# Performance work log

Hardware: AMD Instinct MI355X
Metric: run time of the kernel (lower is better)

Reference implementation:

```python
import jax, jax.numpy as jnp
import numpy as np

N_NODES = 50000
N_EDGES = 800000
IN_DIM = 128
HID_DIM = 128
OUT_DIM = 128
LEAKY_SLOPE = 0.01  # torch F.leaky_relu default


def setup_inputs() -> dict:
    key = jax.random.key(0)
    ks = jax.random.split(key, 10)
    src = jax.random.randint(ks[0], (N_EDGES,), 0, N_NODES)
    dst = jax.random.randint(ks[1], (N_EDGES,), 0, N_NODES)
    x = jax.random.normal(ks[2], (N_NODES, IN_DIM), dtype=jnp.float32)
    mask = jnp.ones((HID_DIM,), dtype=jnp.float32)
    # GraphConv 1 (in -> hid), with bias (DGL default)
    W1 = jax.random.normal(ks[3], (IN_DIM, HID_DIM), dtype=jnp.float32) * (1.0 / np.sqrt(IN_DIM))
    b1 = jnp.zeros((HID_DIM,), dtype=jnp.float32)
    # BicliqueAttentionLayer (hid -> hid), linear has no bias
    Wa = jax.random.normal(ks[4], (HID_DIM, HID_DIM), dtype=jnp.float32) * (1.0 / np.sqrt(HID_DIM))
    a = jax.random.normal(ks[5], (HID_DIM, 1), dtype=jnp.float32) * (1.414 / np.sqrt(HID_DIM))
    # GraphConv 2 (hid -> out)
    W2 = jax.random.normal(ks[6], (HID_DIM, OUT_DIM), dtype=jnp.float32) * (1.0 / np.sqrt(HID_DIM))
    b2 = jnp.zeros((OUT_DIM,), dtype=jnp.float32)
    return {"src": src, "dst": dst, "x": x, "mask": mask,
            "W1": W1, "b1": b1, "Wa": Wa, "a": a, "W2": W2, "b2": b2}


def _inv_sqrt_deg(idx, n):
    deg = jax.ops.segment_sum(jnp.ones(idx.shape[0], jnp.float32), idx, num_segments=n)
    return jnp.where(deg > 0, jax.lax.rsqrt(jnp.maximum(deg, 1.0)), 0.0)


def _graph_conv(h, src, dst, W, b):
    # DGL GraphConv norm='both': D_out^{-1/2} on src side, aggregate, D_in^{-1/2} on dst side
    n = h.shape[0]
    norm_src = _inv_sqrt_deg(src, n)   # out-degree of source nodes
    norm_dst = _inv_sqrt_deg(dst, n)   # in-degree of destination nodes
    h = (h @ W) * norm_src[:, None]    # project first (same math, smaller if out<in)
    agg = jax.ops.segment_sum(h[src], dst, num_segments=n)  # scatter-sum to dst
    return agg * norm_dst[:, None] + b


def _biclique_attn(h, src, dst, mask, Wa, a):
    n = h.shape[0]
    hm = (h * mask[None, :]) @ Wa                      # [N, hid]
    score_node = jnp.squeeze(hm @ a, -1)               # [N] per-node attn logit
    score = jax.nn.leaky_relu(score_node[src], LEAKY_SLOPE)  # [E]
    # segment softmax keyed by dst
    smax = jax.ops.segment_max(score, dst, num_segments=n)   # -inf for empty segments
    e = jnp.exp(score - smax[dst])
    ssum = jax.ops.segment_sum(e, dst, num_segments=n)
    alpha = e / ssum[dst]                              # [E]
    h_new = jax.ops.segment_sum(hm[src] * alpha[:, None], dst, num_segments=n)
    return jax.nn.relu(h_new)


def reference(src, dst, x, mask, W1, b1, Wa, a, W2, b2):
    h = jax.nn.relu(_graph_conv(x, src, dst, W1, b1))
    h = _biclique_attn(h, src, dst, mask, Wa, a)
    h = jax.nn.relu(_graph_conv(h, src, dst, W2, b2))
    return h
```

## Files before the change

kernel.cpp:

```cpp
#include <hip/hip_runtime.h>
#include <hip/hip_fp16.h>
#include <math.h>

#define NNODES 50000
#define NEDGES 800000
#define DIM 128
#define NCOARSE 196
#define SCHUNK 2048
#define KPAD 136
#define BCAP 6144

static inline int ceil_div(int a, int b){ return (a + b - 1) / b; }

__device__ __forceinline__ float leaky01(float x){ return x > 0.f ? x : 0.01f * x; }

typedef _Float16 f16;
typedef f16 f16x4 __attribute__((ext_vector_type(4)));
typedef f16 f16x8 __attribute__((ext_vector_type(8)));
typedef float f32x4 __attribute__((ext_vector_type(4)));

__global__ void waa_init(const float* __restrict__ Wa, const float* __restrict__ a,
                         const float* __restrict__ mask, float* __restrict__ waam,
                         int* __restrict__ dcur, int* __restrict__ scur){
    int gtid = blockIdx.x * blockDim.x + threadIdx.x;
    if (gtid < NCOARSE){ dcur[gtid] = gtid * BCAP; scur[gtid] = gtid * BCAP; }
    int k = gtid >> 6, lane = threadIdx.x & 63;
    if (k >= DIM) return;
    float2 v  = *(const float2*)(Wa + (long long)k * DIM + lane * 2);
    float2 av = *(const float2*)(a + lane * 2);
    float s = fmaf(v.x, av.x, v.y * av.y);
    #pragma unroll
    for (int off = 32; off > 0; off >>= 1) s += __shfl_down(s, off);
    if (lane == 0) waam[k] = s * mask[k];
}

__global__ __launch_bounds__(256) void coarse_scatter(const int* __restrict__ src,
    const int* __restrict__ dst, int* __restrict__ dcur, int* __restrict__ scur,
    int* __restrict__ dbuf, unsigned char* __restrict__ sbuf, int E)
{
    __shared__ int hist[NCOARSE], loff[NCOARSE], gbase[NCOARSE], cur[NCOARSE];
    __shared__ int ws4[4];
    __shared__ int stage[SCHUNK];
    int t = threadIdx.x;
    int lane = t & 63, w = t >> 6;
    int base = blockIdx.x * SCHUNK;
    int lim = base + SCHUNK < E ? base + SCHUNK : E;
    int cnt = lim - base;

    if (t < NCOARSE) hist[t] = 0;
    __syncthreads();
    for (int i = base + t; i < lim; i += 256)
        atomicAdd(&hist[dst[i] >> 8], 1);
    __syncthreads();
    {
        int v = (t < NCOARSE) ? hist[t] : 0;
        int inc = v;
        #pragma unroll
        for (int d = 1; d < 64; d <<= 1){ int u = __shfl_up(inc, d); if (lane >= d) inc += u; }
        if (lane == 63) ws4[w] = inc;
        __syncthreads();
        if (t == 0){ int r = 0;
            #pragma unroll
            for (int k = 0; k < 4; ++k){ int xx = ws4[k]; ws4[k] = r; r += xx; } }
        __syncthreads();
        if (t < NCOARSE){
            int excl = ws4[w] + inc - v;
            loff[t] = excl; cur[t] = excl;
            gbase[t] = v ? atomicAdd(&dcur[t], v) : 0;
        }
    }
    __syncthreads();
    for (int i = base + t; i < lim; i += 256){
        int d = dst[i], s = src[i];
        int b = d >> 8;
        int pos = atomicAdd(&cur[b], 1);
        stage[pos] = (b << 24) | ((d & 255) << 16) | s;
    }
    __syncthreads();
    for (int i = t; i < cnt; i += 256){
        int v = stage[i];
        int b = (int)((unsigned)v >> 24);
        dbuf[gbase[b] + (i - loff[b])] = v;
    }
    __syncthreads();

    if (t < NCOARSE) hist[t] = 0;
    __syncthreads();
    for (int i = base + t; i < lim; i += 256)
        atomicAdd(&hist[src[i] >> 8], 1);
    __syncthreads();
    {
        int v = (t < NCOARSE) ? hist[t] : 0;
        int inc = v;
        #pragma unroll
        for (int d = 1; d < 64; d <<= 1){ int u = __shfl_up(inc, d); if (lane >= d) inc += u; }
        if (lane == 63) ws4[w] = inc;
        __syncthreads();
        if (t == 0){ int r = 0;
            #pragma unroll
            for (int k = 0; k < 4; ++k){ int xx = ws4[k]; ws4[k] = r; r += xx; } }
        __syncthreads();
        if (t < NCOARSE){
            int excl = ws4[w] + inc - v;
            loff[t] = excl; cur[t] = excl;
            gbase[t] = v ? atomicAdd(&scur[t], v) : 0;
        }
    }
    __syncthreads();
    unsigned short* st16 = (unsigned short*)stage;
    for (int i = base + t; i < lim; i += 256){
        int s = src[i];
        int b = s >> 8;
        int pos = atomicAdd(&cur[b], 1);
        st16[pos] = (unsigned short)((b << 8) | (s & 255));
    }
    __syncthreads();
    for (int i = t; i < cnt; i += 256){
        int v = st16[i];
        int b = v >> 8;
        sbuf[gbase[b] + (i - loff[b])] = (unsigned char)(v & 255);
    }
}

__global__ __launch_bounds__(256) void bucket_all(const int* __restrict__ dbuf,
    const unsigned char* __restrict__ sbuf, const int* __restrict__ dcur,
    const int* __restrict__ scur, int* __restrict__ rbeg, int* __restrict__ rend,
    float* __restrict__ nd, float* __restrict__ ns, unsigned short* __restrict__ csrc)
{
    __shared__ int stage[BCAP];
    __shared__ int h[256], off[256], cur[256];
    __shared__ int ws4[4];
    int t = threadIdx.x;
    int b = blockIdx.x;

    if (b < NCOARSE){
        int beg = b * BCAP, end = dcur[b], cnt = end - beg;
        h[t] = 0; cur[t] = 0;
        __syncthreads();
        for (int i = t; i < cnt; i += 256){
            int v = dbuf[beg + i];
            stage[i] = v;
            atomicAdd(&h[(v >> 16) & 255], 1);
        }
        __syncthreads();
        int v = h[t];
        int lane = t & 63, w = t >> 6, inc = v;
        #pragma unroll
        for (int d = 1; d < 64; d <<= 1){
            int u = __shfl_up(inc, d);
            if (lane >= d) inc += u;
        }
        if (lane == 63) ws4[w] = inc;
        __syncthreads();
        if (t == 0){
            int r = 0;
            #pragma unroll
            for (int k = 0; k < 4; ++k){ int xx = ws4[k]; ws4[k] = r; r += xx; }
        }
        __syncthreads();
        off[t] = ws4[w] + inc - v;
        __syncthreads();
        int d = b * 256 + t;
        if (d < NNODES){
            rbeg[d] = beg + off[t];
            rend[d] = beg + off[t] + v;
            nd[d] = v > 0 ? rsqrtf((float)v) : 0.f;
        }
        for (int i = t; i < cnt; i += 256){
            int pv = stage[i];
            int j = (pv >> 16) & 255;
            int pos = atomicAdd(&cur[j], 1);
            csrc[beg + off[j] + pos] = (unsigned short)(pv & 0xFFFF);
        }
    } else {
        b -= NCOARSE;
        int beg = b * BCAP, end = scur[b];
        h[t] = 0;
        __syncthreads();
        for (int i = beg + t; i < end; i += 256)
            atomicAdd(&h[sbuf[i]], 1);
        __syncthreads();
        int s = b * 256 + t;
        if (s < NNODES) ns[s] = h[t] > 0 ? rsqrtf((float)h[t]) : 0.f;
    }
}

template<typename TIN, bool USE_MASK, bool USE_ROWSCALE>
__global__ __launch_bounds__(256) void gemm_mfma(const TIN* __restrict__ in,
    const float* __restrict__ W, const float* __restrict__ mask,
    const float* __restrict__ rowscale, __half* __restrict__ out, int n)
{
    __shared__ f16 Ws[DIM][KPAD];
    __shared__ f16 Xs[64][KPAD];
    const int t = threadIdx.x;

    #pragma unroll
    for (int i = 0; i < 16; ++i){
        int idx = i * 256 + t;
        int c = idx & 127, k0 = (idx >> 7) * 4;
        f16x4 h;
        #pragma unroll
        for (int u = 0; u < 4; ++u){
            float v = W[(long long)(k0 + u) * DIM + c];
            if (USE_MASK) v *= mask[k0 + u];
            h[u] = (f16)v;
        }
        *(f16x4*)&Ws[c][k0] = h;
    }
    const int row0 = blockIdx.x * 64;
    if constexpr (sizeof(TIN) == 4){
        #pragma unroll
        for (int i = 0; i < 8; ++i){
            int idx = i * 256 + t;
            int r = idx >> 5, c4 = (idx & 31) * 4;
            int row = row0 + r;
            float4 v = make_float4(0.f, 0.f, 0.f, 0.f);
            if (row < n) v = *(const float4*)((const float*)in + (long long)row * DIM + c4);
            f16x4 h = { (f16)v.x, (f16)v.y, (f16)v.z, (f16)v.w };
            *(f16x4*)&Xs[r][c4] = h;
        }
    } else {
        #pragma unroll
        for (int i = 0; i < 4; ++i){
            int idx = i * 256 + t;
            int r = idx >> 4, c8 = (idx & 15) * 8;
            int row = row0 + r;
            f16x8 h = { (f16)0, (f16)0, (f16)0, (f16)0, (f16)0, (f16)0, (f16)0, (f16)0 };
            if (row < n) h = *(const f16x8*)((const f16*)in + (long long)row * DIM + c8);
            *(f16x8*)&Xs[r][c8] = h;
        }
    }
    __syncthreads();

    const int lane = t & 63, wid = t >> 6;
    const int l15 = lane & 15, lg = lane >> 4;
    const int wrow = wid * 16;

    f16x8 a[4];
    #pragma unroll
    for (int kc = 0; kc < 4; ++kc)
        a[kc] = *(const f16x8*)&Xs[wrow + l15][kc * 32 + lg * 8];

    float rs[4];
    #pragma unroll
    for (int r = 0; r < 4; ++r){
        int row = row0 + wrow + lg * 4 + r;
        rs[r] = (USE_ROWSCALE && row < n) ? rowscale[row] : 1.f;
    }

    #pragma unroll
    for (int ct = 0; ct < 8; ++ct){
        f32x4 acc = {0.f, 0.f, 0.f, 0.f};
        #pragma unroll
        for (int kc = 0; kc < 4; ++kc){
            f16x8 b = *(const f16x8*)&Ws[ct * 16 + l15][kc * 32 + lg * 8];
            acc = __builtin_amdgcn_mfma_f32_16x16x32_f16(a[kc], b, acc, 0, 0, 0);
        }
        int col = ct * 16 + l15;
        #pragma unroll
        for (int r = 0; r < 4; ++r){
            int row = row0 + wrow + lg * 4 + r;
            if (row < n)
                out[(long long)row * DIM + col] = __float2half(acc[r] * rs[r]);
        }
    }
}

__device__ __forceinline__ void acc8(float* acc, uint4 u, float w){
    float2 f0 = __half22float2(*(__half2*)&u.x);
    float2 f1 = __half22float2(*(__half2*)&u.y);
    float2 f2 = __half22float2(*(__half2*)&u.z);
    float2 f3 = __half22float2(*(__half2*)&u.w);
    acc[0] = fmaf(f0.x, w, acc[0]); acc[1] = fmaf(f0.y, w, acc[1]);
    acc[2] = fmaf(f1.x, w, acc[2]); acc[3] = fmaf(f1.y, w, acc[3]);
    acc[4] = fmaf(f2.x, w, acc[4]); acc[5] = fmaf(f2.y, w, acc[5]);
    acc[6] = fmaf(f3.x, w, acc[6]); acc[7] = fmaf(f3.y, w, acc[7]);
}

template<bool SCORE, typename TOUT>
__global__ __launch_bounds__(256) void agg_conv(const int* __restrict__ rbeg,
    const int* __restrict__ rend, const unsigned short* __restrict__ csrc,
    const __half* __restrict__ p, const float* __restrict__ norm,
    const float* __restrict__ b, const float* __restrict__ waam,
    TOUT* __restrict__ out, float* __restrict__ score, int n)
{
    int wave = (blockIdx.x * blockDim.x + threadIdx.x) >> 6;
    int nwaves = (gridDim.x * blockDim.x) >> 6;
    int lane = threadIdx.x & 63;
    int g = lane >> 4, l16 = lane & 15;

    float4 b0 = *(const float4*)(b + l16 * 8);
    float4 b1 = *(const float4*)(b + l16 * 8 + 4);
    float4 w0, w1;
    if (SCORE){
        w0 = *(const float4*)(waam + l16 * 8);
        w1 = *(const float4*)(waam + l16 * 8 + 4);
    }

    for (int node = wave; node < n; node += nwaves){
        int beg = rbeg[node], end = rend[node];
        float acc[8] = {0.f, 0.f, 0.f, 0.f, 0.f, 0.f, 0.f, 0.f};
        int i = beg + g;
        for (; i + 5 <= end; i += 8){
            int s0 = csrc[i], s1 = csrc[i + 4];
            uint4 u0 = *(const uint4*)(p + (long long)s0 * DIM + l16 * 8);
            uint4 u1 = *(const uint4*)(p + (long long)s1 * DIM + l16 * 8);
            acc8(acc, u0, 1.f);
            acc8(acc, u1, 1.f);
        }
        for (; i < end; i += 4){
            int s = csrc[i];
            uint4 u = *(const uint4*)(p + (long long)s * DIM + l16 * 8);
            acc8(acc, u, 1.f);
        }
        #pragma unroll
        for (int k = 0; k < 8; ++k){
            acc[k] += __shfl_xor(acc[k], 16);
            acc[k] += __shfl_xor(acc[k], 32);
        }
        float nd = norm[node];
        float o[8];
        o[0] = fmaxf(fmaf(acc[0], nd, b0.x), 0.f);
        o[1] = fmaxf(fmaf(acc[1], nd, b0.y), 0.f);
        o[2] = fmaxf(fmaf(acc[2], nd, b0.z), 0.f);
        o[3] = fmaxf(fmaf(acc[3], nd, b0.w), 0.f);
        o[4] = fmaxf(fmaf(acc[4], nd, b1.x), 0.f);
        o[5] = fmaxf(fmaf(acc[5], nd, b1.y), 0.f);
        o[6] = fmaxf(fmaf(acc[6], nd, b1.z), 0.f);
        o[7] = fmaxf(fmaf(acc[7], nd, b1.w), 0.f);
        if (g == 0){
            if constexpr (sizeof(TOUT) == 2){
                __half2 h0 = __floats2half2_rn(o[0], o[1]);
                __half2 h1 = __floats2half2_rn(o[2], o[3]);
                __half2 h2 = __floats2half2_rn(o[4], o[5]);
                __half2 h3 = __floats2half2_rn(o[6], o[7]);
                uint4 u;
                u.x = *(unsigned*)&h0; u.y = *(unsigned*)&h1;
                u.z = *(unsigned*)&h2; u.w = *(unsigned*)&h3;
                *(uint4*)((__half*)out + (long long)node * DIM + l16 * 8) = u;
            } else {
                float* orow = (float*)out + (long long)node * DIM + l16 * 8;
                *(float4*)(orow)     = make_float4(o[0], o[1], o[2], o[3]);
                *(float4*)(orow + 4) = make_float4(o[4], o[5], o[6], o[7]);
            }
        }
        if (SCORE){
            float sc = o[0]*w0.x + o[1]*w0.y + o[2]*w0.z + o[3]*w0.w
                     + o[4]*w1.x + o[5]*w1.y + o[6]*w1.z + o[7]*w1.w;
            #pragma unroll
            for (int d = 1; d < 16; d <<= 1) sc += __shfl_xor(sc, d);
            if (lane == 0) score[node] = sc;
        }
    }
}

__global__ __launch_bounds__(256) void agg_attn(const int* __restrict__ rbeg,
    const int* __restrict__ rend, const unsigned short* __restrict__ csrc,
    const __half* __restrict__ hm, const float* __restrict__ score,
    __half* __restrict__ out, int n)
{
    int wave = (blockIdx.x * blockDim.x + threadIdx.x) >> 6;
    int nwaves = (gridDim.x * blockDim.x) >> 6;
    int lane = threadIdx.x & 63;
    int g = lane >> 4, l16 = lane & 15;

    for (int node = wave; node < n; node += nwaves){
        int beg = rbeg[node], end = rend[node];

        int i0 = beg + lane;
        int s_l = 0; float v_l = -1e30f;
        if (i0 < end){ s_l = csrc[i0]; v_l = leaky01(score[s_l]); }

        float m = v_l;
        for (int i = i0 + 64; i < end; i += 64) m = fmaxf(m, leaky01(score[csrc[i]]));
        #pragma unroll
        for (int off = 32; off > 0; off >>= 1) m = fmaxf(m, __shfl_xor(m, off));

        float w_l = (i0 < end) ? __expf(v_l - m) : 0.f;
        float ss = w_l;
        for (int i = i0 + 64; i < end; i += 64) ss += __expf(leaky01(score[csrc[i]]) - m);
        #pragma unroll
        for (int off = 32; off > 0; off >>= 1) ss += __shfl_xor(ss, off);
        float inv = ss > 0.f ? 1.f / ss : 0.f;

        float acc[8] = {0.f, 0.f, 0.f, 0.f, 0.f, 0.f, 0.f, 0.f};
        {
            int cl = end - beg; if (cl > 64) cl = 64;
            int j4 = 0;
            for (; j4 + 8 <= cl; j4 += 8){
                int jA = j4 + g, jB = j4 + 4 + g;
                float wA = __shfl(w_l, jA), wB = __shfl(w_l, jB);
                int sA = __shfl(s_l, jA), sB = __shfl(s_l, jB);
                uint4 uA = *(const uint4*)(hm + (long long)sA * DIM + l16 * 8);
                uint4 uB = *(const uint4*)(hm + (long long)sB * DIM + l16 * 8);
                acc8(acc, uA, wA);
                acc8(acc, uB, wB);
            }
            for (; j4 < cl; j4 += 4){
                int j = j4 + g;
                int jj = j < cl ? j : 0;
                float w = __shfl(w_l, jj);
                int s = __shfl(s_l, jj);
                if (j < cl){
                    uint4 u = *(const uint4*)(hm + (long long)s * DIM + l16 * 8);
                    acc8(acc, u, w);
                }
            }
        }
        for (int cb = beg + 64; cb < end; cb += 64){
            int cl = end - cb; if (cl > 64) cl = 64;
            int s2 = 0; float w2 = 0.f;
            if (lane < cl){
                s2 = csrc[cb + lane];
                w2 = __expf(leaky01(score[s2]) - m);
            }
            for (int j4 = 0; j4 < cl; j4 += 4){
                int j = j4 + g;
                int jj = j < cl ? j : 0;
                float w = __shfl(w2, jj);
                int s = __shfl(s2, jj);
                if (j < cl){
                    uint4 u = *(const uint4*)(hm + (long long)s * DIM + l16 * 8);
                    acc8(acc, u, w);
                }
            }
        }
        #pragma unroll
        for (int k = 0; k < 8; ++k){
            acc[k] += __shfl_xor(acc[k], 16);
            acc[k] += __shfl_xor(acc[k], 32);
        }
        if (g == 0){
            float o[8];
            #pragma unroll
            for (int k = 0; k < 8; ++k) o[k] = fmaxf(acc[k] * inv, 0.f);
            __half2 h0 = __floats2half2_rn(o[0], o[1]);
            __half2 h1 = __floats2half2_rn(o[2], o[3]);
            __half2 h2 = __floats2half2_rn(o[4], o[5]);
            __half2 h3 = __floats2half2_rn(o[6], o[7]);
            uint4 u;
            u.x = *(unsigned*)&h0; u.y = *(unsigned*)&h1;
            u.z = *(unsigned*)&h2; u.w = *(unsigned*)&h3;
            *(uint4*)(out + (long long)node * DIM + l16 * 8) = u;
        }
    }
}


extern "C" void kernel_launch(void* const* d_in, const int* in_sizes, int n_in,
                              void* d_out, int out_size, void* d_ws, size_t ws_size,
                              hipStream_t stream)
{
    const int*   src  = (const int*)d_in[0];
    const int*   dst  = (const int*)d_in[1];
    const float* x    = (const float*)d_in[2];
    const float* mask = (const float*)d_in[3];
    const float* W1   = (const float*)d_in[4];
    const float* b1   = (const float*)d_in[5];
    const float* Wa   = (const float*)d_in[6];
    const float* a    = (const float*)d_in[7];
    const float* W2   = (const float*)d_in[8];
    const float* b2   = (const float*)d_in[9];
    float* out = (float*)d_out;

    const int N = NNODES, E = NEDGES;
    const long long NB = (long long)N * DIM;
    const long long BSLOTS = (long long)NCOARSE * BCAP;

    __half* bufH     = (__half*)d_ws;
    __half* bufH2    = bufH + NB;
    float*  norm_src = (float*)(bufH2 + NB);
    float*  norm_dst = norm_src + N;
    float*  score    = norm_dst + N;
    float*  waam     = score + N;
    int*    dcur     = (int*)(waam + DIM);
    int*    scur     = dcur + NCOARSE;
    int*    rbeg     = scur + NCOARSE;
    int*    rend     = rbeg + N;
    int*    dbuf     = rend + N;
    unsigned short* csrc = (unsigned short*)(dbuf + BSLOTS);
    unsigned char*  sbuf = (unsigned char*)(csrc + BSLOTS);

    waa_init<<<ceil_div(DIM * 64, 256), 256, 0, stream>>>(Wa, a, mask, waam, dcur, scur);
    coarse_scatter<<<ceil_div(E, SCHUNK), 256, 0, stream>>>(src, dst, dcur, scur, dbuf, sbuf, E);
    bucket_all<<<2 * NCOARSE, 256, 0, stream>>>(dbuf, sbuf, dcur, scur, rbeg, rend,
                                                norm_dst, norm_src, csrc);

    gemm_mfma<float, false, true><<<ceil_div(N, 64), 256, 0, stream>>>(x, W1, nullptr, norm_src, bufH, N);
    agg_conv<true, __half><<<2048, 256, 0, stream>>>(rbeg, rend, csrc, bufH, norm_dst, b1, waam, bufH2, score, N);

    gemm_mfma<__half, true, false><<<ceil_div(N, 64), 256, 0, stream>>>(bufH2, Wa, mask, nullptr, bufH, N);
    agg_attn<<<2048, 256, 0, stream>>>(rbeg, rend, csrc, bufH, score, bufH2, N);

    gemm_mfma<__half, false, true><<<ceil_div(N, 64), 256, 0, stream>>>(bufH2, W2, nullptr, norm_src, bufH, N);
    agg_conv<false, float><<<2048, 256, 0, stream>>>(rbeg, rend, csrc, bufH, norm_dst, b2, nullptr, out, nullptr, N);
}
```

Before: 192.9 us.

## Split feature dimension across XCD halves in aggregation and move score into GEMM

The aggregation kernels now map blocks on XCDs 0-3 to the first 64 feature columns and XCDs 4-7 to the last 64. Each wave handles one node for half the row, with 8-byte gathers and deeper unrolling. The aim is for each XCD's L2 to cache only half of the gathered feature matrix, which improves hit rate for random source gathers. The per-node attention score moves from the first conv aggregation into the Wa GEMM epilogue, computed from the staged input tile in LDS. The cost is that every node's edge list and softmax weights are processed twice (once per half), and the mapping assumes round-robin block-to-XCD dispatch.

```diff
diff --git a/kernel.cpp b/kernel.cpp
--- a/kernel.cpp
+++ b/kernel.cpp
@@ -185,10 +185,11 @@
     }
 }
 
-template<typename TIN, bool USE_MASK, bool USE_ROWSCALE>
+template<typename TIN, bool USE_MASK, bool USE_ROWSCALE, bool SCORE>
 __global__ __launch_bounds__(256) void gemm_mfma(const TIN* __restrict__ in,
     const float* __restrict__ W, const float* __restrict__ mask,
-    const float* __restrict__ rowscale, __half* __restrict__ out, int n)
+    const float* __restrict__ rowscale, const float* __restrict__ waam,
+    float* __restrict__ score, __half* __restrict__ out, int n)
 {
     __shared__ f16 Ws[DIM][KPAD];
     __shared__ f16 Xs[64][KPAD];
@@ -264,92 +265,83 @@
                 out[(long long)row * DIM + col] = __float2half(acc[r] * rs[r]);
         }
     }
-}
-
-__device__ __forceinline__ void acc8(float* acc, uint4 u, float w){
+
+    if (SCORE){
+        int r = t >> 2, q = t & 3;
+        int row = row0 + r;
+        float sc = 0.f;
+        const float* wa = waam + q * 32;
+        #pragma unroll
+        for (int j = 0; j < 32; ++j) sc += (float)Xs[r][q * 32 + j] * wa[j];
+        sc += __shfl_xor(sc, 1);
+        sc += __shfl_xor(sc, 2);
+        if (q == 0 && row < n) score[row] = sc;
+    }
+}
+
+__device__ __forceinline__ void acc4(float* acc, uint2 u, float w){
     float2 f0 = __half22float2(*(__half2*)&u.x);
     float2 f1 = __half22float2(*(__half2*)&u.y);
-    float2 f2 = __half22float2(*(__half2*)&u.z);
-    float2 f3 = __half22float2(*(__half2*)&u.w);
     acc[0] = fmaf(f0.x, w, acc[0]); acc[1] = fmaf(f0.y, w, acc[1]);
     acc[2] = fmaf(f1.x, w, acc[2]); acc[3] = fmaf(f1.y, w, acc[3]);
-    acc[4] = fmaf(f2.x, w, acc[4]); acc[5] = fmaf(f2.y, w, acc[5]);
-    acc[6] = fmaf(f3.x, w, acc[6]); acc[7] = fmaf(f3.y, w, acc[7]);
-}
-
-template<bool SCORE, typename TOUT>
+}
+
+template<typename TOUT>
 __global__ __launch_bounds__(256) void agg_conv(const int* __restrict__ rbeg,
     const int* __restrict__ rend, const unsigned short* __restrict__ csrc,
     const __half* __restrict__ p, const float* __restrict__ norm,
-    const float* __restrict__ b, const float* __restrict__ waam,
-    TOUT* __restrict__ out, float* __restrict__ score, int n)
-{
-    int wave = (blockIdx.x * blockDim.x + threadIdx.x) >> 6;
-    int nwaves = (gridDim.x * blockDim.x) >> 6;
+    const float* __restrict__ b, TOUT* __restrict__ out, int n)
+{
+    int xcd = blockIdx.x & 7;
+    int half = xcd >> 2;
+    int vb = (blockIdx.x >> 3) * 4 + (xcd & 3);
+    int wid = threadIdx.x >> 6;
+    int wave = vb * 4 + wid;
+    int nwaves = gridDim.x << 1;
     int lane = threadIdx.x & 63;
     int g = lane >> 4, l16 = lane & 15;
-
-    float4 b0 = *(const float4*)(b + l16 * 8);
-    float4 b1 = *(const float4*)(b + l16 * 8 + 4);
-    float4 w0, w1;
-    if (SCORE){
-        w0 = *(const float4*)(waam + l16 * 8);
-        w1 = *(const float4*)(waam + l16 * 8 + 4);
-    }
+    int doff = half * 64 + l16 * 4;
+
+    float4 bv = *(const float4*)(b + doff);
 
     for (int node = wave; node < n; node += nwaves){
         int beg = rbeg[node], end = rend[node];
-        float acc[8] = {0.f, 0.f, 0.f, 0.f, 0.f, 0.f, 0.f, 0.f};
+        float acc[4] = {0.f, 0.f, 0.f, 0.f};
         int i = beg + g;
-        for (; i + 5 <= end; i += 8){
-            int s0 = csrc[i], s1 = csrc[i + 4];
-            uint4 u0 = *(const uint4*)(p + (long long)s0 * DIM + l16 * 8);
-            uint4 u1 = *(const uint4*)(p + (long long)s1 * DIM + l16 * 8);
-            acc8(acc, u0, 1.f);
-            acc8(acc, u1, 1.f);
+        for (; i + 13 <= end; i += 16){
+            int s0 = csrc[i], s1 = csrc[i + 4], s2 = csrc[i + 8], s3 = csrc[i + 12];
+            uint2 u0 = *(const uint2*)(p + (long long)s0 * DIM + doff);
+            uint2 u1 = *(const uint2*)(p + (long long)s1 * DIM + doff);
+            uint2 u2 = *(const uint2*)(p + (long long)s2 * DIM + doff);
+            uint2 u3 = *(const uint2*)(p + (long long)s3 * DIM + doff);
+            acc4(acc, u0, 1.f); acc4(acc, u1, 1.f);
+            acc4(acc, u2, 1.f); acc4(acc, u3, 1.f);
         }
         for (; i < end; i += 4){
             int s = csrc[i];
-            uint4 u = *(const uint4*)(p + (long long)s * DIM + l16 * 8);
-            acc8(acc, u, 1.f);
-        }
-        #pragma unroll
-        for (int k = 0; k < 8; ++k){
+            uint2 u = *(const uint2*)(p + (long long)s * DIM + doff);
+            acc4(acc, u, 1.f);
+        }
+        #pragma unroll
+        for (int k = 0; k < 4; ++k){
             acc[k] += __shfl_xor(acc[k], 16);
             acc[k] += __shfl_xor(acc[k], 32);
         }
         float nd = norm[node];
-        float o[8];
-        o[0] = fmaxf(fmaf(acc[0], nd, b0.x), 0.f);
-        o[1] = fmaxf(fmaf(acc[1], nd, b0.y), 0.f);
-        o[2] = fmaxf(fmaf(acc[2], nd, b0.z), 0.f);
-        o[3] = fmaxf(fmaf(acc[3], nd, b0.w), 0.f);
-        o[4] = fmaxf(fmaf(acc[4], nd, b1.x), 0.f);
-        o[5] = fmaxf(fmaf(acc[5], nd, b1.y), 0.f);
-        o[6] = fmaxf(fmaf(acc[6], nd, b1.z), 0.f);
-        o[7] = fmaxf(fmaf(acc[7], nd, b1.w), 0.f);
+        float o0 = fmaxf(fmaf(acc[0], nd, bv.x), 0.f);
+        float o1 = fmaxf(fmaf(acc[1], nd, bv.y), 0.f);
+        float o2 = fmaxf(fmaf(acc[2], nd, bv.z), 0.f);
+        float o3 = fmaxf(fmaf(acc[3], nd, bv.w), 0.f);
         if (g == 0){
             if constexpr (sizeof(TOUT) == 2){
-                __half2 h0 = __floats2half2_rn(o[0], o[1]);
-                __half2 h1 = __floats2half2_rn(o[2], o[3]);
-                __half2 h2 = __floats2half2_rn(o[4], o[5]);
-                __half2 h3 = __floats2half2_rn(o[6], o[7]);
-                uint4 u;
-                u.x = *(unsigned*)&h0; u.y = *(unsigned*)&h1;
-                u.z = *(unsigned*)&h2; u.w = *(unsigned*)&h3;
-                *(uint4*)((__half*)out + (long long)node * DIM + l16 * 8) = u;
+                __half2 h0 = __floats2half2_rn(o0, o1);
+                __half2 h1 = __floats2half2_rn(o2, o3);
+                uint2 u; u.x = *(unsigned*)&h0; u.y = *(unsigned*)&h1;
+                *(uint2*)((__half*)out + (long long)node * DIM + doff) = u;
             } else {
-                float* orow = (float*)out + (long long)node * DIM + l16 * 8;
-                *(float4*)(orow)     = make_float4(o[0], o[1], o[2], o[3]);
-                *(float4*)(orow + 4) = make_float4(o[4], o[5], o[6], o[7]);
+                *(float4*)((float*)out + (long long)node * DIM + doff) =
+                    make_float4(o0, o1, o2, o3);
             }
-        }
-        if (SCORE){
-            float sc = o[0]*w0.x + o[1]*w0.y + o[2]*w0.z + o[3]*w0.w
-                     + o[4]*w1.x + o[5]*w1.y + o[6]*w1.z + o[7]*w1.w;
-            #pragma unroll
-            for (int d = 1; d < 16; d <<= 1) sc += __shfl_xor(sc, d);
-            if (lane == 0) score[node] = sc;
         }
     }
 }
@@ -359,10 +351,15 @@
     const __half* __restrict__ hm, const float* __restrict__ score,
     __half* __restrict__ out, int n)
 {
-    int wave = (blockIdx.x * blockDim.x + threadIdx.x) >> 6;
-    int nwaves = (gridDim.x * blockDim.x) >> 6;
+    int xcd = blockIdx.x & 7;
+    int half = xcd >> 2;
+    int vb = (blockIdx.x >> 3) * 4 + (xcd & 3);
+    int wid = threadIdx.x >> 6;
+    int wave = vb * 4 + wid;
+    int nwaves = gridDim.x << 1;
     int lane = threadIdx.x & 63;
     int g = lane >> 4, l16 = lane & 15;
+    int doff = half * 64 + l16 * 4;
 
     for (int node = wave; node < n; node += nwaves){
         int beg = rbeg[node], end = rend[node];
@@ -383,18 +380,22 @@
         for (int off = 32; off > 0; off >>= 1) ss += __shfl_xor(ss, off);
         float inv = ss > 0.f ? 1.f / ss : 0.f;
 
-        float acc[8] = {0.f, 0.f, 0.f, 0.f, 0.f, 0.f, 0.f, 0.f};
+        float acc[4] = {0.f, 0.f, 0.f, 0.f};
         {
             int cl = end - beg; if (cl > 64) cl = 64;
             int j4 = 0;
-            for (; j4 + 8 <= cl; j4 += 8){
-                int jA = j4 + g, jB = j4 + 4 + g;
+            for (; j4 + 16 <= cl; j4 += 16){
+                int jA = j4 + g, jB = j4 + 4 + g, jC = j4 + 8 + g, jD = j4 + 12 + g;
                 float wA = __shfl(w_l, jA), wB = __shfl(w_l, jB);
+                float wC = __shfl(w_l, jC), wD = __shfl(w_l, jD);
                 int sA = __shfl(s_l, jA), sB = __shfl(s_l, jB);
-                uint4 uA = *(const uint4*)(hm + (long long)sA * DIM + l16 * 8);
-                uint4 uB = *(const uint4*)(hm + (long long)sB * DIM + l16 * 8);
-                acc8(acc, uA, wA);
-                acc8(acc, uB, wB);
+                int sC = __shfl(s_l, jC), sD = __shfl(s_l, jD);
+                uint2 uA = *(const uint2*)(hm + (long long)sA * DIM + doff);
+                uint2 uB = *(const uint2*)(hm + (long long)sB * DIM + doff);
+                uint2 uC = *(const uint2*)(hm + (long long)sC * DIM + doff);
+                uint2 uD = *(const uint2*)(hm + (long long)sD * DIM + doff);
+                acc4(acc, uA, wA); acc4(acc, uB, wB);
+                acc4(acc, uC, wC); acc4(acc, uD, wD);
             }
             for (; j4 < cl; j4 += 4){
                 int j = j4 + g;
@@ -402,8 +403,8 @@
                 float w = __shfl(w_l, jj);
                 int s = __shfl(s_l, jj);
                 if (j < cl){
-                    uint4 u = *(const uint4*)(hm + (long long)s * DIM + l16 * 8);
-                    acc8(acc, u, w);
+                    uint2 u = *(const uint2*)(hm + (long long)s * DIM + doff);
+                    acc4(acc, u, w);
                 }
             }
         }
@@ -420,28 +421,25 @@
                 float w = __shfl(w2, jj);
                 int s = __shfl(s2, jj);
                 if (j < cl){
-                    uint4 u = *(const uint4*)(hm + (long long)s * DIM + l16 * 8);
-                    acc8(acc, u, w);
+                    uint2 u = *(const uint2*)(hm + (long long)s * DIM + doff);
+                    acc4(acc, u, w);
                 }
             }
         }
         #pragma unroll
-        for (int k = 0; k < 8; ++k){
+        for (int k = 0; k < 4; ++k){
             acc[k] += __shfl_xor(acc[k], 16);
             acc[k] += __shfl_xor(acc[k], 32);
         }
         if (g == 0){
-            float o[8];
-            #pragma unroll
-            for (int k = 0; k < 8; ++k) o[k] = fmaxf(acc[k] * inv, 0.f);
-            __half2 h0 = __floats2half2_rn(o[0], o[1]);
-            __half2 h1 = __floats2half2_rn(o[2], o[3]);
-            __half2 h2 = __floats2half2_rn(o[4], o[5]);
-            __half2 h3 = __floats2half2_rn(o[6], o[7]);
-            uint4 u;
-            u.x = *(unsigned*)&h0; u.y = *(unsigned*)&h1;
-            u.z = *(unsigned*)&h2; u.w = *(unsigned*)&h3;
-            *(uint4*)(out + (long long)node * DIM + l16 * 8) = u;
+            float o0 = fmaxf(acc[0] * inv, 0.f);
+            float o1 = fmaxf(acc[1] * inv, 0.f);
+            float o2 = fmaxf(acc[2] * inv, 0.f);
+            float o3 = fmaxf(acc[3] * inv, 0.f);
+            __half2 h0 = __floats2half2_rn(o0, o1);
+            __half2 h1 = __floats2half2_rn(o2, o3);
+            uint2 u; u.x = *(unsigned*)&h0; u.y = *(unsigned*)&h1;
+            *(uint2*)(out + (long long)node * DIM + doff) = u;
         }
     }
 }
@@ -486,12 +484,15 @@
     bucket_all<<<2 * NCOARSE, 256, 0, stream>>>(dbuf, sbuf, dcur, scur, rbeg, rend,
                                                 norm_dst, norm_src, csrc);
 
-    gemm_mfma<float, false, true><<<ceil_div(N, 64), 256, 0, stream>>>(x, W1, nullptr, norm_src, bufH, N);
-    agg_conv<true, __half><<<2048, 256, 0, stream>>>(rbeg, rend, csrc, bufH, norm_dst, b1, waam, bufH2, score, N);
-
-    gemm_mfma<__half, true, false><<<ceil_div(N, 64), 256, 0, stream>>>(bufH2, Wa, mask, nullptr, bufH, N);
+    gemm_mfma<float, false, true, false><<<ceil_div(N, 64), 256, 0, stream>>>(
+        x, W1, nullptr, norm_src, nullptr, nullptr, bufH, N);
+    agg_conv<__half><<<2048, 256, 0, stream>>>(rbeg, rend, csrc, bufH, norm_dst, b1, bufH2, N);
+
+    gemm_mfma<__half, true, false, true><<<ceil_div(N, 64), 256, 0, stream>>>(
+        bufH2, Wa, mask, nullptr, waam, score, bufH, N);
     agg_attn<<<2048, 256, 0, stream>>>(rbeg, rend, csrc, bufH, score, bufH2, N);
 
-    gemm_mfma<__half, false, true><<<ceil_div(N, 64), 256, 0, stream>>>(bufH2, W2, nullptr, norm_src, bufH, N);
-    agg_conv<false, float><<<2048, 256, 0, stream>>>(rbeg, rend, csrc, bufH, norm_dst, b2, nullptr, out, nullptr, N);
-}
+    gemm_mfma<__half, false, true, false><<<ceil_div(N, 64), 256, 0, stream>>>(
+        bufH2, W2, nullptr, norm_src, nullptr, nullptr, bufH, N);
+    agg_conv<float><<<2048, 256, 0, stream>>>(rbeg, rend, csrc, bufH, norm_dst, b2, out, N);
+}
```

Measured after the change: 229.9 us. +19.2%, slower.
